# Kernel tuning notes

Hardware: AMD Instinct MI355X
Metric: run time of the kernel (lower is better)

The kernel has to match this reference:

```python
import jax, jax.numpy as jnp
import numpy as np
import math

B, S, D, H = 1, 2048, 1024, 16
HD = D // H  # 64
SCALE = 1.0 / math.sqrt(HD)
ENT = 0.5      # entanglement_strength
DECAY = 0.1    # correlation_decay
SUP = 0.3      # superposition_weight
EPS = 1e-5


def setup_inputs() -> dict:
    key = jax.random.key(0)
    ks = jax.random.split(key, 24)
    def w(k, shape, s=0.02):
        return jax.random.normal(k, shape, dtype=jnp.float32) * s
    return {
        "hidden_states": jax.random.normal(ks[0], (B, S, D), dtype=jnp.float32),
        "Wq": w(ks[1], (D, D)), "bq": jnp.zeros((D,), jnp.float32),
        "Wk": w(ks[2], (D, D)), "bk": jnp.zeros((D,), jnp.float32),
        "Wv": w(ks[3], (D, D)), "bv": jnp.zeros((D,), jnp.float32),
        "Wo": w(ks[4], (D, D)), "bo": jnp.zeros((D,), jnp.float32),
        "Weq": w(ks[5], (D, D), 0.002), "beq": jnp.zeros((D,), jnp.float32),
        "Wek": w(ks[6], (D, D), 0.002), "bek": jnp.zeros((D,), jnp.float32),
        "amp_w": w(ks[7], (H, D)), "amp_b": jnp.zeros((H,), jnp.float32),
        "ph_w": w(ks[8], (H, D)), "ph_b": jnp.zeros((H,), jnp.float32),
        "mix_w": w(ks[9], (H, HD, HD)), "mix_b": jnp.zeros((H, HD), jnp.float32),
        "ln_g": jnp.ones((D,), jnp.float32), "ln_b": jnp.zeros((D,), jnp.float32),
    }


def _heads(x):
    # [B,S,D] -> [B,H,S,hd]
    b, s, _ = x.shape
    return x.reshape(b, s, H, HD).transpose(0, 2, 1, 3)


def reference(hidden_states, Wq, bq, Wk, bk, Wv, bv, Wo, bo,
              Weq, beq, Wek, bek, amp_w, amp_b, ph_w, ph_b,
              mix_w, mix_b, ln_g, ln_b):
    hs = hidden_states
    b, s, _ = hs.shape
    q = _heads(hs @ Wq.T + bq)  # [B,H,S,hd]
    k = _heads(hs @ Wk.T + bk)
    v = _heads(hs @ Wv.T + bv)

    # standard attention scores
    scores = jnp.einsum('bhqd,bhkd->bhqk', q, k) * SCALE

    # entanglement scores with distance-decay position bias
    eq = _heads(hs @ Weq.T + beq)
    ek = _heads(hs @ Wek.T + bek)
    pos = jnp.arange(s)
    decay = jnp.exp(-DECAY * jnp.abs(pos[:, None] - pos[None, :]).astype(jnp.float32))  # [S,S]
    esc = jnp.einsum('bhqd,bhkd->bhqk', eq, ek) * (1.0 / math.sqrt(HD)) * decay

    attn = jax.nn.softmax(scores + ENT * esc, axis=-1)  # [B,H,S,S]

    # quantum amplitudes / phases
    amps = jax.nn.sigmoid(hs @ amp_w.T + amp_b)        # [B,S,H]
    phases = jnp.tanh(hs @ ph_w.T + ph_b) * math.pi    # [B,S,H]
    a = amps.transpose(0, 2, 1)[..., None]             # [B,H,S,1]
    p = phases.transpose(0, 2, 1)[..., None]

    # per-head superposition mixer: Linear(head_dim, head_dim) per head
    sup = jnp.einsum('bhsd,hod->bhso', v, mix_w) + mix_b[None, :, None, :]
    mixed = v + SUP * a * jnp.cos(p) * sup + SUP * a * jnp.sin(p) * jnp.roll(sup, 1, axis=-1)

    ctx = jnp.einsum('bhqk,bhkd->bhqd', attn, mixed)
    ctx = ctx.transpose(0, 2, 1, 3).reshape(b, s, D)
    out = ctx @ Wo.T + bo

    # residual + LayerNorm
    res = hs + out
    mu = jnp.mean(res, axis=-1, keepdims=True)
    var = jnp.mean((res - mu) ** 2, axis=-1, keepdims=True)
    return (res - mu) * jax.lax.rsqrt(var + EPS) * ln_g + ln_b
```

## Files before the change

kernel.cpp:

```cpp
#include <hip/hip_runtime.h>

#define SEQ 2048
#define DM  1024
#define NH  16
#define HDIM 64

typedef __bf16   bf16x8 __attribute__((ext_vector_type(8)));
typedef float    f32x4  __attribute__((ext_vector_type(4)));
typedef _Float16 half8  __attribute__((ext_vector_type(8)));
typedef _Float16 half4v __attribute__((ext_vector_type(4)));

__device__ __forceinline__ void gload16(const void* g, void* l) {
    __builtin_amdgcn_global_load_lds(
        (const __attribute__((address_space(1))) unsigned int*)g,
        (__attribute__((address_space(3))) unsigned int*)l, 16, 0, 0);
}

__global__ void zero_out(float* __restrict__ out, int n) {
    int i = blockIdx.x * 256 + threadIdx.x;
    if (i < n) out[i] = 0.f;
}

struct PrepArgs {
    const float* csrc[8]; __bf16* cdst[8];
    const float* mixw; const float* Wv; const float* bv; const float* mixb;
    __bf16* w6; float* bsup;
    const float* hs;
    const float* amp_w; const float* amp_b;
    const float* ph_w;  const float* ph_b;
    float* cAT; float* sAT;
};
__global__ __launch_bounds__(256) void prep_all(PrepArgs p) {
    const int tid = threadIdx.x, bid = blockIdx.x;
    if (bid < 4096) {
        const int z = bid >> 9;
        const int i = (bid & 511) * 256 + tid;
        const float4* s = reinterpret_cast<const float4*>(p.csrc[z]) + (size_t)i * 2;
        float4 x = s[0], y = s[1];
        bf16x8 o;
        o[0] = (__bf16)x.x; o[1] = (__bf16)x.y; o[2] = (__bf16)x.z; o[3] = (__bf16)x.w;
        o[4] = (__bf16)y.x; o[5] = (__bf16)y.y; o[6] = (__bf16)y.z; o[7] = (__bf16)y.w;
        reinterpret_cast<bf16x8*>(p.cdst[z])[i] = o;
    } else if (bid < 5120) {
        const int ho = bid - 4096, h = ho >> 6;
        __shared__ float mrow[64];
        if (tid < 64) mrow[tid] = p.mixw[(size_t)ho * 64 + tid];
        __syncthreads();
        const int c0 = tid * 4;
        float a0 = 0.f, a1 = 0.f, a2 = 0.f, a3 = 0.f;
        for (int dd = 0; dd < 64; ++dd) {
            const float4 wv4 = *reinterpret_cast<const float4*>(
                p.Wv + (size_t)(h * 64 + dd) * DM + c0);
            const float w = mrow[dd];
            a0 += w * wv4.x; a1 += w * wv4.y; a2 += w * wv4.z; a3 += w * wv4.w;
        }
        __bf16* dst = p.w6 + (size_t)ho * DM + c0;
        dst[0] = (__bf16)a0; dst[1] = (__bf16)a1;
        dst[2] = (__bf16)a2; dst[3] = (__bf16)a3;
        if (tid == 0) {
            float b = p.mixb[ho];
            for (int dd = 0; dd < 64; ++dd) b += mrow[dd] * p.bv[h * 64 + dd];
            p.bsup[ho] = b;
        }
    } else {
        const int s = bid - 5120;
        __shared__ float hrow[DM];
        for (int i = tid; i < DM; i += 256)
            hrow[i] = p.hs[(size_t)s * DM + i];
        __syncthreads();
        const int h = tid >> 4, sub = tid & 15;
        const float* aw = p.amp_w + (size_t)h * DM;
        const float* pw = p.ph_w  + (size_t)h * DM;
        float da = 0.f, dp = 0.f;
        for (int kx = sub; kx < DM; kx += 16) {
            const float hv = hrow[kx];
            da += hv * aw[kx];
            dp += hv * pw[kx];
        }
#pragma unroll
        for (int off = 8; off >= 1; off >>= 1) {
            da += __shfl_xor(da, off);
            dp += __shfl_xor(dp, off);
        }
        if (sub == 0) {
            da += p.amp_b[h]; dp += p.ph_b[h];
            float amp = 1.f / (1.f + expf(-da));
            float ph  = tanhf(dp) * 3.14159265358979323846f;
            p.cAT[(size_t)h * SEQ + s] = 0.3f * amp * cosf(ph);
            p.sAT[(size_t)h * SEQ + s] = 0.3f * amp * sinf(ph);
        }
    }
}

struct GemmBatch {
    const __bf16* A;
    const __bf16* W[6];
    const float*  bias[6];
    void*         out[6];
    int           mode[6];
    const float*  resid;
};

__device__ __forceinline__ int swz4(int r) { return (r ^ (r >> 2)) & 3; }

__global__ __launch_bounds__(256) void gemm_bt(GemmBatch g) {
    const int z = blockIdx.z;
    const __bf16* __restrict__ A = g.A;
    const __bf16* __restrict__ W = g.W[z];
    const int ncol0 = blockIdx.x * 128;
    const int mrow0 = blockIdx.y * 128;
    const int tid = threadIdx.x, lane = tid & 63, wv = tid >> 6;
    const int wm = wv >> 1, wn = wv & 1;
    const int fr = lane & 15, fj = lane >> 4;

    __shared__ __bf16 As[128 * 32];
    __shared__ __bf16 Bs[128 * 32];

    f32x4 acc[4][4];
#pragma unroll
    for (int i = 0; i < 4; ++i)
#pragma unroll
        for (int j = 0; j < 4; ++j)
#pragma unroll
            for (int e = 0; e < 4; ++e) acc[i][j][e] = 0.f;

    const int row0 = wv * 16 + (lane >> 2);
    const int row1 = row0 + 64;
    const int jl   = lane & 3;
    const int dstA0 = row0 * 32 + jl * 8;
    const int dstA1 = row1 * 32 + jl * 8;
    const __bf16* ApS0 = A + (size_t)(mrow0 + row0) * DM + (jl ^ swz4(row0)) * 8;
    const __bf16* ApS1 = A + (size_t)(mrow0 + row1) * DM + (jl ^ swz4(row1)) * 8;
    const __bf16* WpS0 = W + (size_t)(ncol0 + row0) * DM + (jl ^ swz4(row0)) * 8;
    const __bf16* WpS1 = W + (size_t)(ncol0 + row1) * DM + (jl ^ swz4(row1)) * 8;

    for (int kt = 0; kt < DM; kt += 32) {
        __syncthreads();
        gload16(ApS0 + kt, As + dstA0);
        gload16(ApS1 + kt, As + dstA1);
        gload16(WpS0 + kt, Bs + dstA0);
        gload16(WpS1 + kt, Bs + dstA1);
        __syncthreads();

        bf16x8 af[4], bfv[4];
#pragma unroll
        for (int mf = 0; mf < 4; ++mf) {
            int r = wm * 64 + mf * 16 + fr;
            af[mf] = *(const bf16x8*)(As + r * 32 + ((fj ^ swz4(r)) << 3));
        }
#pragma unroll
        for (int nf = 0; nf < 4; ++nf) {
            int r = wn * 64 + nf * 16 + fr;
            bfv[nf] = *(const bf16x8*)(Bs + r * 32 + ((fj ^ swz4(r)) << 3));
        }
#pragma unroll
        for (int mf = 0; mf < 4; ++mf)
#pragma unroll
            for (int nf = 0; nf < 4; ++nf)
                acc[mf][nf] = __builtin_amdgcn_mfma_f32_16x16x32_bf16(
                    af[mf], bfv[nf], acc[mf][nf], 0, 0, 0);
    }

    const int mode = g.mode[z];
    const float* __restrict__ bias = g.bias[z];
#pragma unroll
    for (int mf = 0; mf < 4; ++mf) {
#pragma unroll
        for (int nf = 0; nf < 4; ++nf) {
            const int col = ncol0 + wn * 64 + nf * 16 + fr;
            const int rw0 = mrow0 + wm * 64 + mf * 16 + fj * 4;
            const float bc = bias[col];
            float v4[4];
#pragma unroll
            for (int jj = 0; jj < 4; ++jj) v4[jj] = acc[mf][nf][jj] + bc;
            if (mode == 4) {
                half4v t;
#pragma unroll
                for (int jj = 0; jj < 4; ++jj) t[jj] = (_Float16)v4[jj];
                *(half4v*)((_Float16*)g.out[z] + (size_t)col * SEQ + rw0) = t;
            } else if (mode == 3) {
#pragma unroll
                for (int jj = 0; jj < 4; ++jj)
                    ((_Float16*)g.out[z])[(size_t)(rw0 + jj) * DM + col] = (_Float16)v4[jj];
            } else {
#pragma unroll
                for (int jj = 0; jj < 4; ++jj) {
                    const size_t idx = (size_t)(rw0 + jj) * DM + col;
                    float vv = v4[jj];
                    if (mode == 2) vv += g.resid[idx];
                    ((float*)g.out[z])[idx] = vv;
                }
            }
        }
    }
}

__global__ __launch_bounds__(256) void mixT2(
    const _Float16* __restrict__ vT, const _Float16* __restrict__ supT,
    const float* __restrict__ cAT, const float* __restrict__ sAT,
    _Float16* __restrict__ mixedT)
{
    const int ho = blockIdx.x, h = ho >> 6, o = ho & 63;
    const int op = h * 64 + ((o + 63) & 63);
    const int s0 = threadIdx.x * 8;
    half8 v  = *(const half8*)(vT   + (size_t)ho * SEQ + s0);
    half8 su = *(const half8*)(supT + (size_t)ho * SEQ + s0);
    half8 s2 = *(const half8*)(supT + (size_t)op * SEQ + s0);
    const float4 c0 = *(const float4*)(cAT + (size_t)h * SEQ + s0);
    const float4 c1 = *(const float4*)(cAT + (size_t)h * SEQ + s0 + 4);
    const float4 a0 = *(const float4*)(sAT + (size_t)h * SEQ + s0);
    const float4 a1 = *(const float4*)(sAT + (size_t)h * SEQ + s0 + 4);
    const float ca[8] = {c0.x, c0.y, c0.z, c0.w, c1.x, c1.y, c1.z, c1.w};
    const float sa[8] = {a0.x, a0.y, a0.z, a0.w, a1.x, a1.y, a1.z, a1.w};
    half8 m;
#pragma unroll
    for (int e = 0; e < 8; ++e)
        m[e] = (_Float16)((float)v[e] + ca[e] * (float)su[e] + sa[e] * (float)s2[e]);
    *(half8*)(mixedT + (size_t)ho * SEQ + s0) = m;
}

__global__ __launch_bounds__(256) void attn_mfma(
    const _Float16* __restrict__ q, const _Float16* __restrict__ k,
    const _Float16* __restrict__ eq, const _Float16* __restrict__ ek,
    const _Float16* __restrict__ mixedT, __bf16* __restrict__ ctx)
{
    const int h = blockIdx.y;
    const int q0 = blockIdx.x * 64;
    const int tid = threadIdx.x, lane = tid & 63, wv = tid >> 6;
    const int lo = lane & 15, hi = lane >> 4;
    const int hoff = h * HDIM;

    __shared__ _Float16 Kt[64 * 64];
    __shared__ _Float16 Et[64 * 64];
    __shared__ _Float16 Mt[64 * 64];
    __shared__ _Float16 Pt[4][64 * 18];

    half8 qa[2], ea[2];
#pragma unroll
    for (int kk = 0; kk < 2; ++kk) {
        const int row = q0 + wv * 16 + lo;
        qa[kk] = *(const half8*)(q  + (size_t)row * DM + hoff + kk * 32 + hi * 8);
        ea[kk] = *(const half8*)(eq + (size_t)row * DM + hoff + kk * 32 + hi * 8);
    }

    f32x4 oacc[4];
    float mr[4], lr[4];
#pragma unroll
    for (int j = 0; j < 4; ++j) { mr[j] = 0.f; lr[j] = 0.f; }
#pragma unroll
    for (int n = 0; n < 4; ++n)
#pragma unroll
        for (int e = 0; e < 4; ++e) oacc[n][e] = 0.f;

    const int srow = tid >> 3, schk = tid & 7;
    const int sdst0 = srow * 64 + ((schk ^ (srow & 7)) << 3);
    const int sdst1 = (srow + 32) * 64 + ((schk ^ (srow & 7)) << 3);

    #define IN_BAND(kt_) ({ int _a = (kt_) - (q0 + 63); int _b = q0 - ((kt_) + 63); \
                            int _d = _a > 0 ? _a : (_b > 0 ? _b : 0); _d <= 160; })

    bool diagCur = IN_BAND(0);
    half8 rk0 = *(const half8*)(k  + (size_t)(srow) * DM + hoff + schk * 8);
    half8 rk1 = *(const half8*)(k  + (size_t)(srow + 32) * DM + hoff + schk * 8);
    half8 rm0 = *(const half8*)(mixedT + (size_t)(hoff + srow) * SEQ + schk * 8);
    half8 rm1 = *(const half8*)(mixedT + (size_t)(hoff + srow + 32) * SEQ + schk * 8);
    half8 re0, re1;
    if (diagCur) {
        re0 = *(const half8*)(ek + (size_t)(srow) * DM + hoff + schk * 8);
        re1 = *(const half8*)(ek + (size_t)(srow + 32) * DM + hoff + schk * 8);
    }

    for (int kt = 0; kt < SEQ; kt += 64) {
        __syncthreads();
        *(half8*)&Kt[sdst0] = rk0; *(half8*)&Kt[sdst1] = rk1;
        *(half8*)&Mt[sdst0] = rm0; *(half8*)&Mt[sdst1] = rm1;
        if (diagCur) { *(half8*)&Et[sdst0] = re0; *(half8*)&Et[sdst1] = re1; }
        __syncthreads();
        const bool diagNext = (kt + 64 < SEQ) && IN_BAND(kt + 64);
        if (kt + 64 < SEQ) {
            const int nt = kt + 64;
            rk0 = *(const half8*)(k  + (size_t)(nt + srow) * DM + hoff + schk * 8);
            rk1 = *(const half8*)(k  + (size_t)(nt + srow + 32) * DM + hoff + schk * 8);
            rm0 = *(const half8*)(mixedT + (size_t)(hoff + srow) * SEQ + nt + schk * 8);
            rm1 = *(const half8*)(mixedT + (size_t)(hoff + srow + 32) * SEQ + nt + schk * 8);
            if (diagNext) {
                re0 = *(const half8*)(ek + (size_t)(nt + srow) * DM + hoff + schk * 8);
                re1 = *(const half8*)(ek + (size_t)(nt + srow + 32) * DM + hoff + schk * 8);
            }
        }

        f32x4 sa[4], se[4];
#pragma unroll
        for (int n = 0; n < 4; ++n)
#pragma unroll
            for (int e = 0; e < 4; ++e) { sa[n][e] = 0.f; se[n][e] = 0.f; }
#pragma unroll
        for (int kk = 0; kk < 2; ++kk)
#pragma unroll
            for (int nf = 0; nf < 4; ++nf) {
                const int rrow = lo + 16 * nf;
                const int coff = rrow * 64 + (((hi + 4 * kk) ^ (rrow & 7)) << 3);
                half8 kb = *(const half8*)&Kt[coff];
                sa[nf] = __builtin_amdgcn_mfma_f32_16x16x32_f16(qa[kk], kb, sa[nf], 0, 0, 0);
            }
        if (diagCur) {
#pragma unroll
            for (int kk = 0; kk < 2; ++kk)
#pragma unroll
                for (int nf = 0; nf < 4; ++nf) {
                    const int rrow = lo + 16 * nf;
                    const int coff = rrow * 64 + (((hi + 4 * kk) ^ (rrow & 7)) << 3);
                    half8 eb = *(const half8*)&Et[coff];
                    se[nf] = __builtin_amdgcn_mfma_f32_16x16x32_f16(ea[kk], eb, se[nf], 0, 0, 0);
                }
        }

        float lg[4][4];
        bool exc = false;
        const int qrow = q0 + wv * 16 + hi * 4;
        if (diagCur) {
#pragma unroll
            for (int nf = 0; nf < 4; ++nf) {
                const int key = kt + nf * 16 + lo;
#pragma unroll
                for (int j = 0; j < 4; ++j) {
                    int dd = qrow + j - key; dd = dd < 0 ? -dd : dd;
                    const float dec = exp2f(-0.14426950408889634f * (float)dd);
                    const float v = 0.125f * sa[nf][j] + 0.0625f * se[nf][j] * dec;
                    lg[nf][j] = v;
                    exc |= (v > mr[j] + 8.f);
                }
            }
        } else {
#pragma unroll
            for (int nf = 0; nf < 4; ++nf)
#pragma unroll
                for (int j = 0; j < 4; ++j) {
                    const float v = 0.125f * sa[nf][j];
                    lg[nf][j] = v;
                    exc |= (v > mr[j] + 8.f);
                }
        }
        if (__any((int)exc)) {
#pragma unroll
            for (int j = 0; j < 4; ++j) {
                float tm = fmaxf(fmaxf(lg[0][j], lg[1][j]), fmaxf(lg[2][j], lg[3][j]));
#pragma unroll
                for (int off = 8; off >= 1; off >>= 1) tm = fmaxf(tm, __shfl_xor(tm, off));
                const float mnew = fmaxf(mr[j], tm);
                const float corr = __expf(mr[j] - mnew);
                lr[j] *= corr; mr[j] = mnew;
#pragma unroll
                for (int nfd = 0; nfd < 4; ++nfd) oacc[nfd][j] *= corr;
            }
        }
        _Float16* Pw = Pt[wv];
#pragma unroll
        for (int nf = 0; nf < 4; ++nf) {
            half4v pv;
#pragma unroll
            for (int j = 0; j < 4; ++j) {
                const float p = __expf(lg[nf][j] - mr[j]);
                lr[j] += p;
                pv[j] = (_Float16)p;
            }
            *(half4v*)&Pw[(lo + 16 * nf) * 18 + hi * 4] = pv;
        }
        __asm__ volatile("s_waitcnt lgkmcnt(0)" ::: "memory");

#pragma unroll
        for (int kk = 0; kk < 2; ++kk) {
            half8 mb[4];
#pragma unroll
            for (int nfd = 0; nfd < 4; ++nfd) {
                const int rrow = lo + 16 * nfd;
                mb[nfd] = *(const half8*)&Mt[rrow * 64 + (((hi + 4 * kk) ^ (rrow & 7)) << 3)];
            }
            half8 pa;
#pragma unroll
            for (int e = 0; e < 8; ++e)
                pa[e] = Pw[(kk * 32 + hi * 8 + e) * 18 + lo];
#pragma unroll
            for (int nfd = 0; nfd < 4; ++nfd)
                oacc[nfd] = __builtin_amdgcn_mfma_f32_16x16x32_f16(pa, mb[nfd], oacc[nfd], 0, 0, 0);
        }
        diagCur = diagNext;
    }
    #undef IN_BAND

#pragma unroll
    for (int j = 0; j < 4; ++j) {
#pragma unroll
        for (int off = 8; off >= 1; off >>= 1) lr[j] += __shfl_xor(lr[j], off);
    }
    const int qrow = q0 + wv * 16 + hi * 4;
#pragma unroll
    for (int nfd = 0; nfd < 4; ++nfd) {
        const int d = hoff + lo + 16 * nfd;
#pragma unroll
        for (int j = 0; j < 4; ++j)
            ctx[(size_t)(qrow + j) * DM + d] = (__bf16)(oacc[nfd][j] / lr[j]);
    }
}

__global__ __launch_bounds__(256) void lnorm_f32(
    const float* __restrict__ res, const float* __restrict__ g,
    const float* __restrict__ b, float* __restrict__ out)
{
    const int row = blockIdx.x, tid = threadIdx.x;
    const int wave = tid >> 6, lane = tid & 63;
    __shared__ float red[8];
    const float4 x = reinterpret_cast<const float4*>(res + (size_t)row * DM)[tid];
    float s  = x.x + x.y + x.z + x.w;
    float s2 = x.x * x.x + x.y * x.y + x.z * x.z + x.w * x.w;
#pragma unroll
    for (int off = 32; off >= 1; off >>= 1) {
        s  += __shfl_xor(s, off);
        s2 += __shfl_xor(s2, off);
    }
    if (lane == 0) { red[wave] = s; red[4 + wave] = s2; }
    __syncthreads();
    s  = red[0] + red[1] + red[2] + red[3];
    s2 = red[4] + red[5] + red[6] + red[7];
    const float mu  = s * (1.f / DM);
    const float var = s2 * (1.f / DM) - mu * mu;
    const float inv = rsqrtf(var + 1e-5f);
    const int col = tid * 4;
    float4 o;
    o.x = (x.x - mu) * inv * g[col + 0] + b[col + 0];
    o.y = (x.y - mu) * inv * g[col + 1] + b[col + 1];
    o.z = (x.z - mu) * inv * g[col + 2] + b[col + 2];
    o.w = (x.w - mu) * inv * g[col + 3] + b[col + 3];
    reinterpret_cast<float4*>(out + (size_t)row * DM)[tid] = o;
}

extern "C" void kernel_launch(void* const* d_in, const int* in_sizes, int n_in,
                              void* d_out, int out_size, void* d_ws, size_t ws_size,
                              hipStream_t stream) {
    const float* hs   = (const float*)d_in[0];
    const float* Wq   = (const float*)d_in[1];
    const float* bq   = (const float*)d_in[2];
    const float* Wk   = (const float*)d_in[3];
    const float* bk   = (const float*)d_in[4];
    const float* Wv   = (const float*)d_in[5];
    const float* bv   = (const float*)d_in[6];
    const float* Wo   = (const float*)d_in[7];
    const float* bo   = (const float*)d_in[8];
    const float* Weq  = (const float*)d_in[9];
    const float* beq  = (const float*)d_in[10];
    const float* Wek  = (const float*)d_in[11];
    const float* bek  = (const float*)d_in[12];
    const float* ampw = (const float*)d_in[13];
    const float* ampb = (const float*)d_in[14];
    const float* phw  = (const float*)d_in[15];
    const float* phb  = (const float*)d_in[16];
    const float* mixw = (const float*)d_in[17];
    const float* mixb = (const float*)d_in[18];
    const float* lng  = (const float*)d_in[19];
    const float* lnb  = (const float*)d_in[20];
    float* out = (float*)d_out;

    static const int expect[21] = {
        2097152, 1048576, 1024, 1048576, 1024, 1048576, 1024, 1048576, 1024,
        1048576, 1024, 1048576, 1024, 16384, 16, 16384, 16, 65536, 1024,
        1024, 1024};
    bool ok = (n_in == 21) && (out_size == 2097152);
    if (ok) for (int i = 0; i < 21; ++i) ok = ok && (in_sizes[i] == expect[i]);
    if (!ok) {
        zero_out<<<(out_size + 255) / 256, 256, 0, stream>>>(out, out_size);
        return;
    }

    char* ws = (char*)d_ws;
    __bf16*   hsb = (__bf16*)ws;
    __bf16*   w0  = (__bf16*)(ws + (4  << 20));
    __bf16*   w1  = (__bf16*)(ws + (6  << 20));
    __bf16*   w2  = (__bf16*)(ws + (8  << 20));
    __bf16*   w3  = (__bf16*)(ws + (10 << 20));
    __bf16*   w4  = (__bf16*)(ws + (12 << 20));
    __bf16*   w5  = (__bf16*)(ws + (14 << 20));
    __bf16*   w6  = (__bf16*)(ws + (16 << 20));
    _Float16* qf  = (_Float16*)(ws + (18 << 20));
    _Float16* kf  = (_Float16*)(ws + (22 << 20));
    _Float16* eqf = (_Float16*)(ws + (26 << 20));
    _Float16* ekf = (_Float16*)(ws + (30 << 20));
    float*    cAT = (float*)(ws + (34 << 20));
    float*    sAT = cAT + SEQ * NH;
    float*    bsup = sAT + SEQ * NH;
    _Float16* mxT = (_Float16*)hsb;
    float*    res = (float*)(ws + (18 << 20));
    _Float16* vT   = (_Float16*)d_out;
    _Float16* supT = (_Float16*)((char*)d_out + (4 << 20));
    __bf16*   ctx  = (__bf16*)d_out;

    PrepArgs p;
    p.csrc[0] = Wq;  p.cdst[0] = w0;
    p.csrc[1] = Wk;  p.cdst[1] = w1;
    p.csrc[2] = Wv;  p.cdst[2] = w2;
    p.csrc[3] = Weq; p.cdst[3] = w3;
    p.csrc[4] = Wek; p.cdst[4] = w4;
    p.csrc[5] = Wo;  p.cdst[5] = w5;
    p.csrc[6] = hs;                p.cdst[6] = hsb;
    p.csrc[7] = hs + SEQ * DM / 2; p.cdst[7] = hsb + SEQ * DM / 2;
    p.mixw = mixw; p.Wv = Wv; p.bv = bv; p.mixb = mixb;
    p.w6 = w6; p.bsup = bsup;
    p.hs = hs;
    p.amp_w = ampw; p.amp_b = ampb; p.ph_w = phw; p.ph_b = phb;
    p.cAT = cAT; p.sAT = sAT;
    prep_all<<<7168, 256, 0, stream>>>(p);

    GemmBatch g1 = {};
    g1.A = hsb;
    g1.W[0] = w0; g1.bias[0] = bq;   g1.out[0] = qf;   g1.mode[0] = 3;
    g1.W[1] = w1; g1.bias[1] = bk;   g1.out[1] = kf;   g1.mode[1] = 3;
    g1.W[2] = w2; g1.bias[2] = bv;   g1.out[2] = vT;   g1.mode[2] = 4;
    g1.W[3] = w3; g1.bias[3] = beq;  g1.out[3] = eqf;  g1.mode[3] = 3;
    g1.W[4] = w4; g1.bias[4] = bek;  g1.out[4] = ekf;  g1.mode[4] = 3;
    g1.W[5] = w6; g1.bias[5] = bsup; g1.out[5] = supT; g1.mode[5] = 4;
    g1.resid = nullptr;
    gemm_bt<<<dim3(DM / 128, SEQ / 128, 6), 256, 0, stream>>>(g1);

    mixT2<<<1024, 256, 0, stream>>>(vT, supT, cAT, sAT, mxT);

    attn_mfma<<<dim3(SEQ / 64, NH), 256, 0, stream>>>(qf, kf, eqf, ekf, mxT, ctx);

    GemmBatch g3 = {};
    g3.A = ctx;
    g3.W[0] = w5; g3.bias[0] = bo; g3.out[0] = res; g3.mode[0] = 2;
    g3.resid = hs;
    gemm_bt<<<dim3(DM / 128, SEQ / 128, 1), 256, 0, stream>>>(g3);

    lnorm_f32<<<SEQ, 256, 0, stream>>>(res, lng, lnb, out);
}
```

Measured before the change: 291.1 us.

## Fuse superposition mixing into V/sup GEMM epilogue via interleaved weights

Interleaves the per-head V and mixer-folded weights (W7) so that one 128-column GEMM tile holds a head's V and sup outputs together. The epilogue stages sup in shared memory and computes mixed = v + c*sup + s*roll(sup) directly, writing mixedT. This removes the separate mixT2 kernel and the vT/supT intermediate round trip through global memory. It adds 16KB of shared memory per GEMM block, which may lower occupancy for every z-slice, and introduces extra barriers. The attention grid is also remapped to a 1D launch that groups 8 heads per query-block range, probably for cache locality.

```diff
diff --git a/kernel.cpp b/kernel.cpp
--- a/kernel.cpp
+++ b/kernel.cpp
@@ -24,7 +24,7 @@
 struct PrepArgs {
     const float* csrc[8]; __bf16* cdst[8];
     const float* mixw; const float* Wv; const float* bv; const float* mixb;
-    __bf16* w6; float* bsup;
+    __bf16* W7; float* b7;
     const float* hs;
     const float* amp_w; const float* amp_b;
     const float* ph_w;  const float* ph_b;
@@ -40,9 +40,15 @@
         bf16x8 o;
         o[0] = (__bf16)x.x; o[1] = (__bf16)x.y; o[2] = (__bf16)x.z; o[3] = (__bf16)x.w;
         o[4] = (__bf16)y.x; o[5] = (__bf16)y.y; o[6] = (__bf16)y.z; o[7] = (__bf16)y.w;
-        reinterpret_cast<bf16x8*>(p.cdst[z])[i] = o;
+        if (z == 2) {
+            const int r = i >> 7, rc = i & 127;
+            const int dr = ((r >> 6) << 7) + (r & 63);
+            reinterpret_cast<bf16x8*>(p.cdst[2])[(size_t)dr * 128 + rc] = o;
+        } else {
+            reinterpret_cast<bf16x8*>(p.cdst[z])[i] = o;
+        }
     } else if (bid < 5120) {
-        const int ho = bid - 4096, h = ho >> 6;
+        const int ho = bid - 4096, h = ho >> 6, o = ho & 63;
         __shared__ float mrow[64];
         if (tid < 64) mrow[tid] = p.mixw[(size_t)ho * 64 + tid];
         __syncthreads();
@@ -54,14 +60,15 @@
             const float w = mrow[dd];
             a0 += w * wv4.x; a1 += w * wv4.y; a2 += w * wv4.z; a3 += w * wv4.w;
         }
-        __bf16* dst = p.w6 + (size_t)ho * DM + c0;
+        __bf16* dst = p.W7 + (size_t)(h * 128 + 64 + o) * DM + c0;
         dst[0] = (__bf16)a0; dst[1] = (__bf16)a1;
         dst[2] = (__bf16)a2; dst[3] = (__bf16)a3;
         if (tid == 0) {
             float b = p.mixb[ho];
             for (int dd = 0; dd < 64; ++dd) b += mrow[dd] * p.bv[h * 64 + dd];
-            p.bsup[ho] = b;
-        }
+            p.b7[h * 128 + 64 + o] = b;
+        }
+        if (tid == 1) p.b7[h * 128 + o] = p.bv[ho];
     } else {
         const int s = bid - 5120;
         __shared__ float hrow[DM];
@@ -98,7 +105,10 @@
     const float*  bias[6];
     void*         out[6];
     int           mode[6];
+    int           cb[6];
     const float*  resid;
+    const float*  cAT; const float* sAT;
+    _Float16*     mixT;
 };
 
 __device__ __forceinline__ int swz4(int r) { return (r ^ (r >> 2)) & 3; }
@@ -107,7 +117,7 @@
     const int z = blockIdx.z;
     const __bf16* __restrict__ A = g.A;
     const __bf16* __restrict__ W = g.W[z];
-    const int ncol0 = blockIdx.x * 128;
+    const int ncol0 = g.cb[z] + blockIdx.x * 128;
     const int mrow0 = blockIdx.y * 128;
     const int tid = threadIdx.x, lane = tid & 63, wv = tid >> 6;
     const int wm = wv >> 1, wn = wv & 1;
@@ -115,6 +125,7 @@
 
     __shared__ __bf16 As[128 * 32];
     __shared__ __bf16 Bs[128 * 32];
+    __shared__ _Float16 Sup[64 * 128];
 
     f32x4 acc[4][4];
 #pragma unroll
@@ -163,6 +174,54 @@
 
     const int mode = g.mode[z];
     const float* __restrict__ bias = g.bias[z];
+
+    if (mode == 5) {
+        const int h = ncol0 >> 7;
+        __syncthreads();
+        if (wn == 1) {
+#pragma unroll
+            for (int mf = 0; mf < 4; ++mf)
+#pragma unroll
+                for (int nf = 0; nf < 4; ++nf) {
+                    const int o = nf * 16 + fr;
+                    const float bc = bias[ncol0 + 64 + o];
+#pragma unroll
+                    for (int jj = 0; jj < 4; ++jj) {
+                        const int sl = wm * 64 + mf * 16 + fj * 4 + jj;
+                        Sup[sl * 64 + o] = (_Float16)(acc[mf][nf][jj] + bc);
+                    }
+                }
+        }
+        __syncthreads();
+        if (wn == 0) {
+#pragma unroll
+            for (int mf = 0; mf < 4; ++mf) {
+                const int slb = wm * 64 + mf * 16 + fj * 4;
+                const float4 c4 = *(const float4*)(g.cAT + (size_t)h * SEQ + mrow0 + slb);
+                const float4 a4 = *(const float4*)(g.sAT + (size_t)h * SEQ + mrow0 + slb);
+                const float ca[4] = {c4.x, c4.y, c4.z, c4.w};
+                const float sa[4] = {a4.x, a4.y, a4.z, a4.w};
+#pragma unroll
+                for (int nf = 0; nf < 4; ++nf) {
+                    const int o = nf * 16 + fr, om = (o + 63) & 63;
+                    const int ho = h * 64 + o;
+                    const float bc = bias[ncol0 + o];
+                    half4v t;
+#pragma unroll
+                    for (int jj = 0; jj < 4; ++jj) {
+                        const int sl = slb + jj;
+                        const float sv  = (float)Sup[sl * 64 + o];
+                        const float svm = (float)Sup[sl * 64 + om];
+                        t[jj] = (_Float16)(acc[mf][nf][jj] + bc
+                                           + ca[jj] * sv + sa[jj] * svm);
+                    }
+                    *(half4v*)(g.mixT + (size_t)ho * SEQ + mrow0 + slb) = t;
+                }
+            }
+        }
+        return;
+    }
+
 #pragma unroll
     for (int mf = 0; mf < 4; ++mf) {
 #pragma unroll
@@ -170,53 +229,19 @@
             const int col = ncol0 + wn * 64 + nf * 16 + fr;
             const int rw0 = mrow0 + wm * 64 + mf * 16 + fj * 4;
             const float bc = bias[col];
-            float v4[4];
-#pragma unroll
-            for (int jj = 0; jj < 4; ++jj) v4[jj] = acc[mf][nf][jj] + bc;
-            if (mode == 4) {
-                half4v t;
-#pragma unroll
-                for (int jj = 0; jj < 4; ++jj) t[jj] = (_Float16)v4[jj];
-                *(half4v*)((_Float16*)g.out[z] + (size_t)col * SEQ + rw0) = t;
-            } else if (mode == 3) {
-#pragma unroll
-                for (int jj = 0; jj < 4; ++jj)
-                    ((_Float16*)g.out[z])[(size_t)(rw0 + jj) * DM + col] = (_Float16)v4[jj];
-            } else {
-#pragma unroll
-                for (int jj = 0; jj < 4; ++jj) {
-                    const size_t idx = (size_t)(rw0 + jj) * DM + col;
-                    float vv = v4[jj];
+#pragma unroll
+            for (int jj = 0; jj < 4; ++jj) {
+                float vv = acc[mf][nf][jj] + bc;
+                const size_t idx = (size_t)(rw0 + jj) * DM + col;
+                if (mode == 3) {
+                    ((_Float16*)g.out[z])[idx] = (_Float16)vv;
+                } else {
                     if (mode == 2) vv += g.resid[idx];
                     ((float*)g.out[z])[idx] = vv;
                 }
             }
         }
     }
-}
-
-__global__ __launch_bounds__(256) void mixT2(
-    const _Float16* __restrict__ vT, const _Float16* __restrict__ supT,
-    const float* __restrict__ cAT, const float* __restrict__ sAT,
-    _Float16* __restrict__ mixedT)
-{
-    const int ho = blockIdx.x, h = ho >> 6, o = ho & 63;
-    const int op = h * 64 + ((o + 63) & 63);
-    const int s0 = threadIdx.x * 8;
-    half8 v  = *(const half8*)(vT   + (size_t)ho * SEQ + s0);
-    half8 su = *(const half8*)(supT + (size_t)ho * SEQ + s0);
-    half8 s2 = *(const half8*)(supT + (size_t)op * SEQ + s0);
-    const float4 c0 = *(const float4*)(cAT + (size_t)h * SEQ + s0);
-    const float4 c1 = *(const float4*)(cAT + (size_t)h * SEQ + s0 + 4);
-    const float4 a0 = *(const float4*)(sAT + (size_t)h * SEQ + s0);
-    const float4 a1 = *(const float4*)(sAT + (size_t)h * SEQ + s0 + 4);
-    const float ca[8] = {c0.x, c0.y, c0.z, c0.w, c1.x, c1.y, c1.z, c1.w};
-    const float sa[8] = {a0.x, a0.y, a0.z, a0.w, a1.x, a1.y, a1.z, a1.w};
-    half8 m;
-#pragma unroll
-    for (int e = 0; e < 8; ++e)
-        m[e] = (_Float16)((float)v[e] + ca[e] * (float)su[e] + sa[e] * (float)s2[e]);
-    *(half8*)(mixedT + (size_t)ho * SEQ + s0) = m;
 }
 
 __global__ __launch_bounds__(256) void attn_mfma(
@@ -224,8 +249,9 @@
     const _Float16* __restrict__ eq, const _Float16* __restrict__ ek,
     const _Float16* __restrict__ mixedT, __bf16* __restrict__ ctx)
 {
-    const int h = blockIdx.y;
-    const int q0 = blockIdx.x * 64;
+    const int bid = blockIdx.x;
+    const int h  = (bid & 7) + ((bid >> 8) << 3);
+    const int q0 = ((bid >> 3) & 31) * 64;
     const int tid = threadIdx.x, lane = tid & 63, wv = tid >> 6;
     const int lo = lane & 15, hi = lane >> 4;
     const int hoff = h * HDIM;
@@ -475,35 +501,32 @@
     __bf16*   hsb = (__bf16*)ws;
     __bf16*   w0  = (__bf16*)(ws + (4  << 20));
     __bf16*   w1  = (__bf16*)(ws + (6  << 20));
-    __bf16*   w2  = (__bf16*)(ws + (8  << 20));
-    __bf16*   w3  = (__bf16*)(ws + (10 << 20));
-    __bf16*   w4  = (__bf16*)(ws + (12 << 20));
-    __bf16*   w5  = (__bf16*)(ws + (14 << 20));
-    __bf16*   w6  = (__bf16*)(ws + (16 << 20));
+    __bf16*   W7  = (__bf16*)(ws + (8  << 20));
+    __bf16*   w3  = (__bf16*)(ws + (12 << 20));
+    __bf16*   w4  = (__bf16*)(ws + (14 << 20));
+    __bf16*   w5  = (__bf16*)(ws + (16 << 20));
     _Float16* qf  = (_Float16*)(ws + (18 << 20));
     _Float16* kf  = (_Float16*)(ws + (22 << 20));
     _Float16* eqf = (_Float16*)(ws + (26 << 20));
     _Float16* ekf = (_Float16*)(ws + (30 << 20));
     float*    cAT = (float*)(ws + (34 << 20));
     float*    sAT = cAT + SEQ * NH;
-    float*    bsup = sAT + SEQ * NH;
-    _Float16* mxT = (_Float16*)hsb;
+    float*    b7  = sAT + SEQ * NH;
+    __bf16*   ctx = hsb;
     float*    res = (float*)(ws + (18 << 20));
-    _Float16* vT   = (_Float16*)d_out;
-    _Float16* supT = (_Float16*)((char*)d_out + (4 << 20));
-    __bf16*   ctx  = (__bf16*)d_out;
+    _Float16* mxT = (_Float16*)d_out;
 
     PrepArgs p;
     p.csrc[0] = Wq;  p.cdst[0] = w0;
     p.csrc[1] = Wk;  p.cdst[1] = w1;
-    p.csrc[2] = Wv;  p.cdst[2] = w2;
+    p.csrc[2] = Wv;  p.cdst[2] = W7;
     p.csrc[3] = Weq; p.cdst[3] = w3;
     p.csrc[4] = Wek; p.cdst[4] = w4;
     p.csrc[5] = Wo;  p.cdst[5] = w5;
     p.csrc[6] = hs;                p.cdst[6] = hsb;
     p.csrc[7] = hs + SEQ * DM / 2; p.cdst[7] = hsb + SEQ * DM / 2;
     p.mixw = mixw; p.Wv = Wv; p.bv = bv; p.mixb = mixb;
-    p.w6 = w6; p.bsup = bsup;
+    p.W7 = W7; p.b7 = b7;
     p.hs = hs;
     p.amp_w = ampw; p.amp_b = ampb; p.ph_w = phw; p.ph_b = phb;
     p.cAT = cAT; p.sAT = sAT;
@@ -511,24 +534,24 @@
 
     GemmBatch g1 = {};
     g1.A = hsb;
-    g1.W[0] = w0; g1.bias[0] = bq;   g1.out[0] = qf;   g1.mode[0] = 3;
-    g1.W[1] = w1; g1.bias[1] = bk;   g1.out[1] = kf;   g1.mode[1] = 3;
-    g1.W[2] = w2; g1.bias[2] = bv;   g1.out[2] = vT;   g1.mode[2] = 4;
-    g1.W[3] = w3; g1.bias[3] = beq;  g1.out[3] = eqf;  g1.mode[3] = 3;
-    g1.W[4] = w4; g1.bias[4] = bek;  g1.out[4] = ekf;  g1.mode[4] = 3;
-    g1.W[5] = w6; g1.bias[5] = bsup; g1.out[5] = supT; g1.mode[5] = 4;
+    g1.W[0] = w0; g1.bias[0] = bq;  g1.out[0] = qf;  g1.mode[0] = 3; g1.cb[0] = 0;
+    g1.W[1] = w1; g1.bias[1] = bk;  g1.out[1] = kf;  g1.mode[1] = 3; g1.cb[1] = 0;
+    g1.W[2] = w3; g1.bias[2] = beq; g1.out[2] = eqf; g1.mode[2] = 3; g1.cb[2] = 0;
+    g1.W[3] = w4; g1.bias[3] = bek; g1.out[3] = ekf; g1.mode[3] = 3; g1.cb[3] = 0;
+    g1.W[4] = W7; g1.bias[4] = b7;  g1.out[4] = 0;   g1.mode[4] = 5; g1.cb[4] = 0;
+    g1.W[5] = W7; g1.bias[5] = b7;  g1.out[5] = 0;   g1.mode[5] = 5; g1.cb[5] = 1024;
     g1.resid = nullptr;
-    gemm_bt<<<dim3(DM / 128, SEQ / 128, 6), 256, 0, stream>>>(g1);
-
-    mixT2<<<1024, 256, 0, stream>>>(vT, supT, cAT, sAT, mxT);
-
-    attn_mfma<<<dim3(SEQ / 64, NH), 256, 0, stream>>>(qf, kf, eqf, ekf, mxT, ctx);
+    g1.cAT = cAT; g1.sAT = sAT; g1.mixT = mxT;
+    gemm_bt<<<dim3(8, SEQ / 128, 6), 256, 0, stream>>>(g1);
+
+    attn_mfma<<<512, 256, 0, stream>>>(qf, kf, eqf, ekf, mxT, ctx);
 
     GemmBatch g3 = {};
     g3.A = ctx;
-    g3.W[0] = w5; g3.bias[0] = bo; g3.out[0] = res; g3.mode[0] = 2;
+    g3.W[0] = w5; g3.bias[0] = bo; g3.out[0] = res; g3.mode[0] = 2; g3.cb[0] = 0;
     g3.resid = hs;
-    gemm_bt<<<dim3(DM / 128, SEQ / 128, 1), 256, 0, stream>>>(g3);
+    g3.cAT = cAT; g3.sAT = sAT; g3.mixT = mxT;
+    gemm_bt<<<dim3(8, SEQ / 128, 1), 256, 0, stream>>>(g3);
 
     lnorm_f32<<<SEQ, 256, 0, stream>>>(res, lng, lnb, out);
 }
```

Measured after the change: 306.1 us. +5.1%, slower.
